# Optimization experiments

Measured on AMD Instinct MI355X. Metric: run time of the kernel, lower is better.

## Reference

```python
import jax, jax.numpy as jnp
import numpy as np

EMBED_DIM = 768
NUM_HEADS = 12
HEAD_DIM = EMBED_DIM // NUM_HEADS
SCALE = HEAD_DIM ** -0.5


def setup_inputs() -> dict:
    key = jax.random.key(0)
    k_x, k_qw, k_qb, k_pw, k_pb = jax.random.split(key, 5)
    B, N, C = 8, 1024, EMBED_DIM
    std = C ** -0.5
    return {
        "x": jax.random.normal(k_x, (B, N, C), dtype=jnp.float32),
        "qkv_w": jax.random.normal(k_qw, (C, 3 * C), dtype=jnp.float32) * std,
        "qkv_b": jax.random.normal(k_qb, (3 * C,), dtype=jnp.float32) * 0.02,
        "proj_w": jax.random.normal(k_pw, (C, C), dtype=jnp.float32) * std,
        "proj_b": jax.random.normal(k_pb, (C,), dtype=jnp.float32) * 0.02,
    }


def reference(x, qkv_w, qkv_b, proj_w, proj_b):
    B, N, C = x.shape
    # QKV projection: [B,N,3C] -> [3,B,H,N,Dh]
    qkv = (x @ qkv_w + qkv_b).reshape(B, N, 3, NUM_HEADS, HEAD_DIM)
    qkv = jnp.transpose(qkv, (2, 0, 3, 1, 4))
    q, k, v = qkv[0], qkv[1], qkv[2]
    # attention scores [B,H,N,N]
    attn = jnp.einsum("bhqd,bhkd->bhqk", q, k) * SCALE
    attn_weights = jax.nn.softmax(attn, axis=-1)
    # dropout=0.0 (eval) -> identity
    out = jnp.einsum("bhqk,bhkd->bhqd", attn_weights, v)
    out = jnp.transpose(out, (0, 2, 1, 3)).reshape(B, N, C)
    out = out @ proj_w + proj_b
    return out, attn_weights
```

## Files before the change

kernel.cpp:

```cpp
#include <hip/hip_runtime.h>
#include <cstdint>
#include <cstddef>

namespace {

constexpr int B = 8, NSEQ = 1024, C = 768, H = 12, D = 64, N3 = 2304;
constexpr float SCALE = 0.125f;
constexpr size_t QKV_ELEMS = (size_t)B * H * NSEQ * D;

using f32x4 = __attribute__((ext_vector_type(4))) float;
using s16x8 = __attribute__((ext_vector_type(8))) short;

__device__ __forceinline__ unsigned short f2bf(float f) {
  union { float f; uint32_t u; } v; v.f = f;
  const uint32_t r = v.u + 0x7FFFu + ((v.u >> 16) & 1u);
  return (unsigned short)(r >> 16);
}
__device__ __forceinline__ float bf2f(unsigned short s) {
  union { uint32_t u; float f; } v; v.u = ((uint32_t)s) << 16;
  return v.f;
}
__device__ __forceinline__ void gload_lds16(const void* g, void* l) {
  __builtin_amdgcn_global_load_lds(
      (const __attribute__((address_space(1))) uint32_t*)g,
      (__attribute__((address_space(3))) uint32_t*)l, 16, 0, 0);
}

__global__ __launch_bounds__(256)
void cvt_x(const float* __restrict__ x, unsigned short* __restrict__ xb, int n4) {
  const int stride = gridDim.x * 256;
  for (int idx = blockIdx.x * 256 + threadIdx.x; idx < n4; idx += stride) {
    const float4 v = ((const float4*)x)[idx];
    ushort4 o;
    o.x = f2bf(v.x); o.y = f2bf(v.y); o.z = f2bf(v.z); o.w = f2bf(v.w);
    ((ushort4*)xb)[idx] = o;
  }
}

__global__ __launch_bounds__(256)
void transp_cvt(const float* __restrict__ w, unsigned short* __restrict__ wt,
                int K, int N) {
  __shared__ float t[32][33];
  const int n0 = blockIdx.x << 5, k0 = blockIdx.y << 5;
  const int tid = threadIdx.x;
  #pragma unroll
  for (int r = 0; r < 4; ++r) {
    const int e = (r << 8) + tid;
    const int kk = e >> 5, nn = e & 31;
    t[kk][nn] = w[(size_t)(k0 + kk) * N + n0 + nn];
  }
  __syncthreads();
  #pragma unroll
  for (int r = 0; r < 4; ++r) {
    const int e = (r << 8) + tid;
    const int nn = e >> 5, kk = e & 31;
    wt[(size_t)(n0 + nn) * K + k0 + kk] = f2bf(t[kk][nn]);
  }
}

template<int MODE>
__global__ __launch_bounds__(256, 2)
void gemm_bf16(const unsigned short* __restrict__ A,
               const unsigned short* __restrict__ Wt,
               const float* __restrict__ bias,
               unsigned short* __restrict__ qp, unsigned short* __restrict__ kp,
               unsigned short* __restrict__ vt, float* __restrict__ out32,
               int N, int NT) {
  constexpr int K = 768;
  __shared__ short As[128 * 64];
  __shared__ short Bs[128 * 64];
  const int tid = threadIdx.x;
  const int wid = tid >> 6, lane = tid & 63;
  const int wm = wid >> 1, wn = wid & 1;
  const int lg = lane >> 4, lr = lane & 15;

  const int cpx = gridDim.x >> 3;
  const int logical = (blockIdx.x & 7) * cpx + (blockIdx.x >> 3);
  const int bx = logical % NT, by = logical / NT;
  const int m0 = by << 7, n0 = bx << 7;

  f32x4 acc[4][4] = {};

  for (int k0 = 0; k0 < K; k0 += 64) {
    __syncthreads();
    #pragma unroll
    for (int r = 0; r < 4; ++r) {
      const int c = (r << 8) + tid;
      const int row = c >> 3, g8 = c & 7;
      const int gp = g8 ^ (row & 7);
      const int ldsoff = (((r << 8) + (wid << 6)) << 3);
      gload_lds16(A + (size_t)(m0 + row) * K + k0 + (gp << 3), (void*)(As + ldsoff));
      gload_lds16(Wt + (size_t)(n0 + row) * K + k0 + (gp << 3), (void*)(Bs + ldsoff));
    }
    __syncthreads();
    #pragma unroll
    for (int kc = 0; kc < 2; ++kc) {
      s16x8 af[4], bf[4];
      #pragma unroll
      for (int i = 0; i < 4; ++i) {
        const int ra = (wm << 6) + (i << 4) + lr;
        const int ca = ((kc << 2) + lg) ^ (ra & 7);
        af[i] = *(const s16x8*)(As + (ra << 6) + (ca << 3));
        const int rb = (wn << 6) + (i << 4) + lr;
        const int cb = ((kc << 2) + lg) ^ (rb & 7);
        bf[i] = *(const s16x8*)(Bs + (rb << 6) + (cb << 3));
      }
      #pragma unroll
      for (int i = 0; i < 4; ++i)
        #pragma unroll
        for (int j = 0; j < 4; ++j)
          acc[i][j] = __builtin_amdgcn_mfma_f32_16x16x32_bf16(af[i], bf[j], acc[i][j], 0, 0, 0);
    }
  }

  #pragma unroll
  for (int i = 0; i < 4; ++i) {
    const int m = m0 + (wm << 6) + (i << 4) + (lg << 2);
    #pragma unroll
    for (int j = 0; j < 4; ++j) {
      const int n = n0 + (wn << 6) + (j << 4) + lr;
      const float bv = bias[n];
      if (MODE == 0) {
        const int which = (n >= 1536) ? 2 : (n >= 768 ? 1 : 0);
        const int hh = (n - which * 768) >> 6;
        const int d = n & 63;
        const int b = m >> 10, ns = m & 1023;
        const size_t bh = (size_t)b * H + hh;
        if (which < 2) {
          unsigned short* dst = (which == 0 ? qp : kp) + (bh * NSEQ + ns) * D + d;
          #pragma unroll
          for (int rg = 0; rg < 4; ++rg)
            dst[(size_t)rg * D] = f2bf(acc[i][j][rg] + bv);
        } else {
          ushort4 pk;
          pk.x = f2bf(acc[i][j][0] + bv);
          pk.y = f2bf(acc[i][j][1] + bv);
          pk.z = f2bf(acc[i][j][2] + bv);
          pk.w = f2bf(acc[i][j][3] + bv);
          *(ushort4*)(vt + (bh * D + d) * NSEQ + ns) = pk;
        }
      } else {
        float* dst = out32 + (size_t)m * N + n;
        #pragma unroll
        for (int rg = 0; rg < 4; ++rg)
          dst[(size_t)rg * N] = acc[i][j][rg] + bv;
      }
    }
  }
}

constexpr int RS = 1032;

__global__ __launch_bounds__(512, 4)
void attn_mfma(const unsigned short* __restrict__ qg,
               const unsigned short* __restrict__ kg,
               const unsigned short* __restrict__ vtg,
               float* __restrict__ attnw,
               unsigned short* __restrict__ aout) {
  __shared__ short sc[32][RS];
  __shared__ short kv[64 * 64];
  __shared__ float invs[32];
  const int tid = threadIdx.x;
  const int wid = tid >> 6, lane = tid & 63;
  const int lg = lane >> 4, lr = lane & 15;
  const int wq = wid >> 2, ws = wid & 3;

  const int logical = (blockIdx.x & 7) * 384 + (blockIdx.x >> 3);
  const int bh = logical >> 5;
  const int q0 = (logical & 31) << 5;
  const size_t kvbase = (size_t)bh * NSEQ * D;

  s16x8 qf[2];
  #pragma unroll
  for (int kc = 0; kc < 2; ++kc)
    qf[kc] = *(const s16x8*)(qg + kvbase + (size_t)(q0 + (wq << 4) + lr) * D + (kc << 5) + (lg << 3));

  for (int j0 = 0; j0 < NSEQ; j0 += 64) {
    __syncthreads();
    {
      const int row = tid >> 3, g8 = tid & 7;
      gload_lds16(kg + kvbase + (size_t)(j0 + row) * D + ((g8 ^ (row & 7)) << 3),
                  (void*)(kv + (wid << 9)));
    }
    __syncthreads();
    f32x4 cacc = {};
    const int krow = (ws << 4) + lr;
    #pragma unroll
    for (int kc = 0; kc < 2; ++kc) {
      const int cg = ((kc << 2) + lg) ^ (krow & 7);
      const s16x8 kf = *(const s16x8*)(kv + (krow << 6) + (cg << 3));
      cacc = __builtin_amdgcn_mfma_f32_16x16x32_bf16(qf[kc], kf, cacc, 0, 0, 0);
    }
    const int jg = j0 + (ws << 4) + lr;
    #pragma unroll
    for (int rg = 0; rg < 4; ++rg)
      sc[(wq << 4) + (lg << 2) + rg][jg] = (short)f2bf(cacc[rg] * SCALE);
  }
  __syncthreads();

  {
    const int row = tid >> 4, ql = tid & 15;
    float mx = -3.0e38f;
    #pragma unroll
    for (int c = 0; c < 8; ++c) {
      const s16x8 v = *(const s16x8*)(&sc[row][(ql << 3) + (c << 7)]);
      #pragma unroll
      for (int e = 0; e < 8; ++e) mx = fmaxf(mx, bf2f((unsigned short)v[e]));
    }
    #pragma unroll
    for (int off = 8; off > 0; off >>= 1) mx = fmaxf(mx, __shfl_xor(mx, off, 16));
    float s = 0.f;
    #pragma unroll
    for (int c = 0; c < 8; ++c) {
      s16x8 v = *(s16x8*)(&sc[row][(ql << 3) + (c << 7)]);
      #pragma unroll
      for (int e = 0; e < 8; ++e) {
        const float ev = __expf(bf2f((unsigned short)v[e]) - mx);
        s += ev;
        v[e] = (short)f2bf(ev);
      }
      *(s16x8*)(&sc[row][(ql << 3) + (c << 7)]) = v;
    }
    #pragma unroll
    for (int off = 8; off > 0; off >>= 1) s += __shfl_xor(s, off, 16);
    if (ql == 0) invs[row] = 1.0f / s;
  }
  __syncthreads();

  f32x4 oacc = {};
  for (int j0 = 0; j0 < NSEQ; j0 += 64) {
    __syncthreads();
    {
      const int row = tid >> 3, g8 = tid & 7;
      gload_lds16(vtg + (size_t)bh * D * NSEQ + (size_t)row * NSEQ + j0 + ((g8 ^ (row & 7)) << 3),
                  (void*)(kv + (wid << 9)));
    }
    __syncthreads();
    const int drow = (ws << 4) + lr;
    #pragma unroll
    for (int kc = 0; kc < 2; ++kc) {
      const s16x8 pa = *(const s16x8*)(&sc[(wq << 4) + lr][j0 + (kc << 5) + (lg << 3)]);
      const int cg = ((kc << 2) + lg) ^ (drow & 7);
      const s16x8 vf = *(const s16x8*)(kv + (drow << 6) + (cg << 3));
      oacc = __builtin_amdgcn_mfma_f32_16x16x32_bf16(pa, vf, oacc, 0, 0, 0);
    }
  }

  {
    const int b = bh / H, hh = bh - b * H;
    const int d = (ws << 4) + lr;
    #pragma unroll
    for (int rg = 0; rg < 4; ++rg) {
      const int qi = (wq << 4) + (lg << 2) + rg;
      aout[((size_t)b * NSEQ + q0 + qi) * C + hh * D + d] = f2bf(oacc[rg] * invs[qi]);
    }
  }

  {
    float* wbase = attnw + ((size_t)bh * NSEQ + q0) * NSEQ;
    #pragma unroll
    for (int r = 0; r < 8; ++r) {
      const int row = (r << 2) + (tid >> 7);
      const int colb = (tid & 127) << 3;
      const float iv = invs[row];
      const s16x8 e8 = *(const s16x8*)(&sc[row][colb]);
      float4 o0, o1;
      o0.x = bf2f((unsigned short)e8[0]) * iv; o0.y = bf2f((unsigned short)e8[1]) * iv;
      o0.z = bf2f((unsigned short)e8[2]) * iv; o0.w = bf2f((unsigned short)e8[3]) * iv;
      o1.x = bf2f((unsigned short)e8[4]) * iv; o1.y = bf2f((unsigned short)e8[5]) * iv;
      o1.z = bf2f((unsigned short)e8[6]) * iv; o1.w = bf2f((unsigned short)e8[7]) * iv;
      *(float4*)(wbase + (size_t)row * NSEQ + colb) = o0;
      *(float4*)(wbase + (size_t)row * NSEQ + colb + 4) = o1;
    }
  }
}

}

extern "C" void kernel_launch(void* const* d_in, const int* in_sizes, int n_in,
                              void* d_out, int out_size, void* d_ws, size_t ws_size,
                              hipStream_t stream) {
  const float* x      = (const float*)d_in[0];
  const float* qkv_w  = (const float*)d_in[1];
  const float* qkv_b  = (const float*)d_in[2];
  const float* proj_w = (const float*)d_in[3];
  const float* proj_b = (const float*)d_in[4];

  float* out   = (float*)d_out;
  float* attnw = out + (size_t)B * NSEQ * C;

  unsigned short* xb   = (unsigned short*)d_ws;
  unsigned short* wtq  = xb   + (size_t)8192 * 768;
  unsigned short* wtp  = wtq  + (size_t)2304 * 768;
  unsigned short* qp   = wtp  + (size_t)768 * 768;
  unsigned short* kp   = qp   + QKV_ELEMS;
  unsigned short* vtp  = kp   + QKV_ELEMS;
  unsigned short* wsao = vtp  + QKV_ELEMS;

  cvt_x<<<1024, 256, 0, stream>>>(x, xb, (int)((size_t)8192 * 768 / 4));
  transp_cvt<<<dim3(N3 / 32, C / 32), 256, 0, stream>>>(qkv_w, wtq, C, N3);
  transp_cvt<<<dim3(C / 32, C / 32), 256, 0, stream>>>(proj_w, wtp, C, C);

  gemm_bf16<0><<<(N3 / 128) * (8192 / 128), 256, 0, stream>>>(
      xb, wtq, qkv_b, qp, kp, vtp, nullptr, N3, N3 / 128);

  attn_mfma<<<(NSEQ / 32) * (B * H), 512, 0, stream>>>(qp, kp, vtp, attnw, wsao);

  gemm_bf16<1><<<(C / 128) * (8192 / 128), 256, 0, stream>>>(
      wsao, wtp, proj_b, nullptr, nullptr, nullptr, out, C, C / 128);
}
```

Measured before the change: 283.8 us.

## Load K and V fragments directly from global memory, drop LDS staging and barriers

The attention kernel no longer stages K and V tiles through shared memory with two barriers per 64-column step. Each wave now reads its MFMA operand fragments straight from global memory, relying on L1/L2 reuse across the waves of a block. The PV loop uses two independent accumulators to give the MFMA chain more instruction-level parallelism. The attention-weight stores become nontemporal to avoid polluting the cache. Redundant global reads across waves could raise cache traffic in exchange for removing synchronisation.

```diff
diff --git a/kernel.cpp b/kernel.cpp
--- a/kernel.cpp
+++ b/kernel.cpp
@@ -158,7 +158,6 @@
                float* __restrict__ attnw,
                unsigned short* __restrict__ aout) {
   __shared__ short sc[32][RS];
-  __shared__ short kv[64 * 64];
   __shared__ float invs[32];
   const int tid = threadIdx.x;
   const int wid = tid >> 6, lane = tid & 63;
@@ -175,26 +174,21 @@
   for (int kc = 0; kc < 2; ++kc)
     qf[kc] = *(const s16x8*)(qg + kvbase + (size_t)(q0 + (wq << 4) + lr) * D + (kc << 5) + (lg << 3));
 
-  for (int j0 = 0; j0 < NSEQ; j0 += 64) {
-    __syncthreads();
-    {
-      const int row = tid >> 3, g8 = tid & 7;
-      gload_lds16(kg + kvbase + (size_t)(j0 + row) * D + ((g8 ^ (row & 7)) << 3),
-                  (void*)(kv + (wid << 9)));
-    }
-    __syncthreads();
-    f32x4 cacc = {};
-    const int krow = (ws << 4) + lr;
-    #pragma unroll
-    for (int kc = 0; kc < 2; ++kc) {
-      const int cg = ((kc << 2) + lg) ^ (krow & 7);
-      const s16x8 kf = *(const s16x8*)(kv + (krow << 6) + (cg << 3));
-      cacc = __builtin_amdgcn_mfma_f32_16x16x32_bf16(qf[kc], kf, cacc, 0, 0, 0);
-    }
-    const int jg = j0 + (ws << 4) + lr;
-    #pragma unroll
-    for (int rg = 0; rg < 4; ++rg)
-      sc[(wq << 4) + (lg << 2) + rg][jg] = (short)f2bf(cacc[rg] * SCALE);
+  {
+    const unsigned short* kptr = kg + kvbase + (size_t)((ws << 4) + lr) * D + (lg << 3);
+    #pragma unroll 4
+    for (int t = 0; t < 16; ++t) {
+      f32x4 cacc = {};
+      #pragma unroll
+      for (int kc = 0; kc < 2; ++kc) {
+        const s16x8 kf = *(const s16x8*)(kptr + t * 64 * D + (kc << 5));
+        cacc = __builtin_amdgcn_mfma_f32_16x16x32_bf16(qf[kc], kf, cacc, 0, 0, 0);
+      }
+      const int jg = (t << 6) + (ws << 4) + lr;
+      #pragma unroll
+      for (int rg = 0; rg < 4; ++rg)
+        sc[(wq << 4) + (lg << 2) + rg][jg] = (short)f2bf(cacc[rg] * SCALE);
+    }
   }
   __syncthreads();
 
@@ -227,22 +221,21 @@
   }
   __syncthreads();
 
-  f32x4 oacc = {};
-  for (int j0 = 0; j0 < NSEQ; j0 += 64) {
-    __syncthreads();
-    {
-      const int row = tid >> 3, g8 = tid & 7;
-      gload_lds16(vtg + (size_t)bh * D * NSEQ + (size_t)row * NSEQ + j0 + ((g8 ^ (row & 7)) << 3),
-                  (void*)(kv + (wid << 9)));
-    }
-    __syncthreads();
-    const int drow = (ws << 4) + lr;
-    #pragma unroll
-    for (int kc = 0; kc < 2; ++kc) {
-      const s16x8 pa = *(const s16x8*)(&sc[(wq << 4) + lr][j0 + (kc << 5) + (lg << 3)]);
-      const int cg = ((kc << 2) + lg) ^ (drow & 7);
-      const s16x8 vf = *(const s16x8*)(kv + (drow << 6) + (cg << 3));
-      oacc = __builtin_amdgcn_mfma_f32_16x16x32_bf16(pa, vf, oacc, 0, 0, 0);
+  f32x4 oa0 = {}, oa1 = {};
+  {
+    const unsigned short* vptr = vtg + kvbase + (size_t)((ws << 4) + lr) * NSEQ + (lg << 3);
+    const short* prow = &sc[(wq << 4) + lr][lg << 3];
+    #pragma unroll 2
+    for (int t = 0; t < 8; ++t) {
+      #pragma unroll
+      for (int kc = 0; kc < 2; ++kc) {
+        const s16x8 va = *(const s16x8*)(vptr + (t << 7) + (kc << 5));
+        const s16x8 pa = *(const s16x8*)(prow + (t << 7) + (kc << 5));
+        oa0 = __builtin_amdgcn_mfma_f32_16x16x32_bf16(pa, va, oa0, 0, 0, 0);
+        const s16x8 vb = *(const s16x8*)(vptr + (t << 7) + 64 + (kc << 5));
+        const s16x8 pb = *(const s16x8*)(prow + (t << 7) + 64 + (kc << 5));
+        oa1 = __builtin_amdgcn_mfma_f32_16x16x32_bf16(pb, vb, oa1, 0, 0, 0);
+      }
     }
   }
 
@@ -252,7 +245,8 @@
     #pragma unroll
     for (int rg = 0; rg < 4; ++rg) {
       const int qi = (wq << 4) + (lg << 2) + rg;
-      aout[((size_t)b * NSEQ + q0 + qi) * C + hh * D + d] = f2bf(oacc[rg] * invs[qi]);
+      aout[((size_t)b * NSEQ + q0 + qi) * C + hh * D + d] =
+          f2bf((oa0[rg] + oa1[rg]) * invs[qi]);
     }
   }
 
@@ -264,13 +258,13 @@
       const int colb = (tid & 127) << 3;
       const float iv = invs[row];
       const s16x8 e8 = *(const s16x8*)(&sc[row][colb]);
-      float4 o0, o1;
-      o0.x = bf2f((unsigned short)e8[0]) * iv; o0.y = bf2f((unsigned short)e8[1]) * iv;
-      o0.z = bf2f((unsigned short)e8[2]) * iv; o0.w = bf2f((unsigned short)e8[3]) * iv;
-      o1.x = bf2f((unsigned short)e8[4]) * iv; o1.y = bf2f((unsigned short)e8[5]) * iv;
-      o1.z = bf2f((unsigned short)e8[6]) * iv; o1.w = bf2f((unsigned short)e8[7]) * iv;
-      *(float4*)(wbase + (size_t)row * NSEQ + colb) = o0;
-      *(float4*)(wbase + (size_t)row * NSEQ + colb + 4) = o1;
+      f32x4 o0, o1;
+      o0[0] = bf2f((unsigned short)e8[0]) * iv; o0[1] = bf2f((unsigned short)e8[1]) * iv;
+      o0[2] = bf2f((unsigned short)e8[2]) * iv; o0[3] = bf2f((unsigned short)e8[3]) * iv;
+      o1[0] = bf2f((unsigned short)e8[4]) * iv; o1[1] = bf2f((unsigned short)e8[5]) * iv;
+      o1[2] = bf2f((unsigned short)e8[6]) * iv; o1[3] = bf2f((unsigned short)e8[7]) * iv;
+      __builtin_nontemporal_store(o0, (f32x4*)(wbase + (size_t)row * NSEQ + colb));
+      __builtin_nontemporal_store(o1, (f32x4*)(wbase + (size_t)row * NSEQ + colb + 4));
     }
   }
 }
```

New measurement: 292.4 us. +3.0%, slower.
